# Optimization experiments

Measured on AMD Instinct MI355X. Metric: run time of the kernel, lower is better.

Reference implementation:

```python
import jax, jax.numpy as jnp
import numpy as np

N, E = 50000, 800000
NODE_IN, EDGE_IN, HID, OUT = 64, 16, 64, 32
BN_EPS = 1e-5


def _linear_params(key, fan_in, fan_out):
    kw, kb = jax.random.split(key)
    lim = 1.0 / np.sqrt(fan_in)
    W = jax.random.uniform(kw, (fan_in, fan_out), minval=-lim, maxval=lim, dtype=jnp.float32)
    b = jax.random.uniform(kb, (fan_out,), minval=-lim, maxval=lim, dtype=jnp.float32)
    return W, b


def setup_inputs() -> dict:
    key = jax.random.key(0)
    ks = jax.random.split(key, 8)
    x = jax.random.normal(ks[0], (N, NODE_IN), dtype=jnp.float32)
    edge_index = jax.random.randint(ks[1], (2, E), 0, N, dtype=jnp.int64)
    edge_attr = jax.random.normal(ks[2], (E, EDGE_IN), dtype=jnp.float32)
    # layer 1: message Linear(node_in + edge_in -> hid), self Linear(node_in -> hid)
    W1_msg, b1_msg = _linear_params(ks[3], NODE_IN + EDGE_IN, HID)
    W1_self, b1_self = _linear_params(ks[4], NODE_IN, HID)
    # BatchNorm1d(hidden) params (inference mode: running stats)
    bn_gamma = jnp.ones((HID,), jnp.float32)
    bn_beta = jnp.zeros((HID,), jnp.float32)
    bn_mean = jax.random.normal(ks[5], (HID,), dtype=jnp.float32) * 0.1
    bn_var = jax.random.uniform(ks[6], (HID,), minval=0.5, maxval=1.5, dtype=jnp.float32)
    # layer 2: message Linear(hid + edge_in -> out), self Linear(hid -> out)
    k7, k8 = jax.random.split(ks[7])
    W2_msg, b2_msg = _linear_params(k7, HID + EDGE_IN, OUT)
    W2_self, b2_self = _linear_params(k8, HID, OUT)
    return dict(x=x, edge_index=edge_index, edge_attr=edge_attr,
                W1_msg=W1_msg, b1_msg=b1_msg, W1_self=W1_self, b1_self=b1_self,
                bn_gamma=bn_gamma, bn_beta=bn_beta, bn_mean=bn_mean, bn_var=bn_var,
                W2_msg=W2_msg, b2_msg=b2_msg, W2_self=W2_self, b2_self=b2_self)


def _gnn_layer(x, edge_index, edge_attr, W_msg, b_msg, W_self, b_self):
    # gather source node features per edge, concat edge features, linear, scatter-sum to dst
    src, dst = edge_index[0], edge_index[1]
    m = jnp.concatenate([x[src], edge_attr], axis=-1) @ W_msg + b_msg  # [E, out]
    agg = jax.ops.segment_sum(m, dst, num_segments=x.shape[0])          # [N, out]
    return x @ W_self + b_self + agg


def reference(x, edge_index, edge_attr,
              W1_msg, b1_msg, W1_self, b1_self,
              bn_gamma, bn_beta, bn_mean, bn_var,
              W2_msg, b2_msg, W2_self, b2_self):
    h = _gnn_layer(x, edge_index, edge_attr, W1_msg, b1_msg, W1_self, b1_self)
    # BatchNorm1d (eval mode, running stats) + ReLU; dropout is identity in eval
    h = (h - bn_mean) * jax.lax.rsqrt(bn_var + BN_EPS) * bn_gamma + bn_beta
    h = jax.nn.relu(h)
    return _gnn_layer(h, edge_index, edge_attr, W2_msg, b2_msg, W2_self, b2_self)
```

## Files before the change

kernel.cpp:

```cpp
#include <hip/hip_runtime.h>

#define NN 50000
#define NE 800000
#define NB 6250
#define NT 3125
#define SCB 49
#define NBK 128
#define BNODE 391
#define BCAP 7680
#define SCAP 56

typedef __attribute__((ext_vector_type(8))) short short8x;
typedef __attribute__((ext_vector_type(4))) float f32x4;

#define OFF_CNT   0LL
#define OFF_ROW   ((long long)NN)
#define OFF_RECS  (3LL*NN + 16)
#define OFF_FLAGS (35LL*NN + 16)
#define OFF_BS    (35LL*NN + 32)
#define OFF_BO    (35LL*NN + 96)
#define OFF_PK    (35LL*NN + 160)
#define OFF_FB1S  (35LL*NN + 7840)
#define OFF_FB2S  (35LL*NN + 7904)
#define OFF_F1    (36LL*NN)
#define OFF_F2    (116LL*NN)
#define OFF_Y2B   (164LL*NN)
#define OFF_S2    (180LL*NN)
#define OFF_BCUR  (212LL*NN)

__device__ __forceinline__ float ldf(const void* p, long long i, int bf16) {
  if (bf16) {
    unsigned short u = ((const unsigned short*)p)[i];
    return __uint_as_float(((unsigned)u) << 16);
  }
  return ((const float*)p)[i];
}
__device__ __forceinline__ unsigned short f2bf(float f) {
  unsigned u = __float_as_uint(f);
  unsigned r = (u + 0x7fffu + ((u >> 16) & 1u)) >> 16;
  return (unsigned short)r;
}
__device__ __forceinline__ unsigned pk2(float lo, float hi) {
  return (unsigned)f2bf(lo) | ((unsigned)f2bf(hi) << 16);
}
__device__ __forceinline__ int ldidx(const void* p, long long i, int i64) {
  return i64 ? (int)((const long long*)p)[i] : ((const int*)p)[i];
}
__device__ __forceinline__ float bflo(unsigned u) { return __uint_as_float(u << 16); }
__device__ __forceinline__ float bfhi(unsigned u) { return __uint_as_float(u & 0xffff0000u); }

__global__ void k_detect(const void* ei, const void* x, int* flags) {
  int lane = threadIdx.x & 63;
  const int* p = (const int*)ei;
  int any = 0;
  for (int i = lane; i < 256; i += 64) any |= p[2 * i + 1];
  unsigned long long anyb = __ballot(any != 0);
  const unsigned short* q = (const unsigned short*)x;
  int cnt = 0;
  for (int i = lane; i < 256; i += 64) {
    unsigned short w = q[2 * i];
    int e = (w >> 7) & 0xff;
    if (w == 0 || (e >= 110 && e <= 140)) cnt++;
  }
  for (int m = 1; m < 64; m <<= 1) cnt += __shfl_xor(cnt, m, 64);
  if (lane == 0) {
    flags[0] = (anyb == 0ull) ? 1 : 0;
    flags[1] = (cnt >= 192) ? 1 : 0;
  }
}

__global__ __launch_bounds__(256) void k_prep(
    const void* __restrict__ W1_msg, const void* __restrict__ b1_msg,
    const void* __restrict__ W1_self, const void* __restrict__ b1_self,
    const void* __restrict__ gamma, const void* __restrict__ beta,
    const void* __restrict__ mean, const void* __restrict__ var,
    const void* __restrict__ W2_msg, const void* __restrict__ b2_msg,
    const void* __restrict__ W2_self, const void* __restrict__ b2_self,
    const int* __restrict__ flags, unsigned short* __restrict__ PK,
    float* __restrict__ fb1s, float* __restrict__ fb2s) {
  int bf = flags[1];
  int t0 = blockIdx.x * 256 + threadIdx.x;
  int stride = gridDim.x * 256;
  for (int i = t0; i < 10240; i += stride) {
    int j = i & 7, L = (i >> 3) & 63, t = (i >> 9) & 3, c = i >> 11;
    int k = c * 32 + ((L >> 4) << 3) + j;
    int col = t * 16 + (L & 15);
    float sc = ldf(gamma, col, bf) * rsqrtf(ldf(var, col, bf) + 1e-5f);
    float v;
    if (k < 64) v = ldf(W1_msg, k * 64 + col, bf) * sc;
    else if (k < 128) v = ldf(W1_self, (k - 64) * 64 + col, bf) * sc;
    else if (k < 144) v = ldf(W1_msg, (64 + k - 128) * 64 + col, bf) * sc;
    else if (k == 144) v = ldf(b1_msg, col, bf) * sc;
    else v = 0.0f;
    PK[i] = f2bf(v);
  }
  for (int i = t0; i < 2048; i += stride) {
    int j = i & 7, L = (i >> 3) & 63, t = (i >> 9) & 1, c = i >> 10;
    int k = c * 32 + ((L >> 4) << 3) + j;
    int col = t * 16 + (L & 15);
    PK[10240 + i] = f2bf(ldf(W2_msg, k * 32 + col, bf));
  }
  for (int i = t0; i < 3072; i += stride) {
    int j = i & 7, L = (i >> 3) & 63, t = (i >> 9) & 1, c = i >> 10;
    int k = c * 32 + ((L >> 4) << 3) + j;
    int col = t * 16 + (L & 15);
    float v;
    if (k < 64) v = ldf(W2_self, k * 32 + col, bf);
    else if (k < 80) v = ldf(W2_msg, k * 32 + col, bf);
    else if (k == 80) v = ldf(b2_msg, col, bf);
    else v = 0.0f;
    PK[12288 + i] = f2bf(v);
  }
  for (int i = t0; i < 64; i += stride) {
    float sc = ldf(gamma, i, bf) * rsqrtf(ldf(var, i, bf) + 1e-5f);
    fb1s[i] = ldf(b1_self, i, bf) * sc + ldf(beta, i, bf) - ldf(mean, i, bf) * sc;
  }
  for (int i = t0; i < 32; i += stride) fb2s[i] = ldf(b2_self, i, bf);
}

__global__ __launch_bounds__(256) void k_bin(const void* __restrict__ ei,
                                             const int* __restrict__ flags,
                                             int* __restrict__ bcur,
                                             int2* __restrict__ binbuf) {
  __shared__ int2 stage[NBK][SCAP];
  __shared__ int scnt[NBK];
  __shared__ int gbase[NBK];
  int tid = threadIdx.x;
  for (int i = tid; i < NBK; i += 256) scnt[i] = 0;
  __syncthreads();
  int i64 = flags[0];
  for (long long e0 = (long long)blockIdx.x * 256; e0 < NE;
       e0 += (long long)gridDim.x * 256) {
    long long e = e0 + tid;
    if (e < NE) {
      int src = ldidx(ei, e, i64);
      int dst = ldidx(ei, NE + e, i64);
      int b = dst / BNODE;
      int dl = dst - b * BNODE;
      int2 ent = make_int2(src | (dl << 16), (int)e);
      int pos = atomicAdd(&scnt[b], 1);
      if (pos < SCAP) {
        stage[b][pos] = ent;
      } else {
        int gp = atomicAdd(&bcur[b], 1);
        binbuf[(long long)b * BCAP + gp] = ent;
      }
    }
  }
  __syncthreads();
  if (tid < NBK) {
    int cb = scnt[tid] < SCAP ? scnt[tid] : SCAP;
    gbase[tid] = atomicAdd(&bcur[tid], cb);
  }
  __syncthreads();
  for (int b = 0; b < NBK; ++b) {
    int cb = scnt[b] < SCAP ? scnt[b] : SCAP;
    for (int i = tid; i < cb; i += 256)
      binbuf[(long long)b * BCAP + gbase[b] + i] = stage[b][i];
  }
}

__global__ __launch_bounds__(256) void k_bhist(const int* __restrict__ bcur,
                                               const int2* __restrict__ binbuf,
                                               int* __restrict__ counts) {
  __shared__ int lh[BNODE];
  int b = blockIdx.x;
  int tid = threadIdx.x;
  for (int i = tid; i < BNODE; i += 256) lh[i] = 0;
  __syncthreads();
  int cnt = bcur[b];
  for (int i = tid; i < cnt; i += 256) {
    int dl = (binbuf[(long long)b * BCAP + i].x >> 16) & 0x3FF;
    atomicAdd(&lh[dl], 1);
  }
  __syncthreads();
  int base = b * BNODE;
  int nn = NN - base < BNODE ? NN - base : BNODE;
  for (int i = tid; i < nn; i += 256) counts[base + i] = lh[i];
}

__global__ __launch_bounds__(1024) void k_scanA(const int* __restrict__ counts,
                                                int* __restrict__ bs) {
  __shared__ int sd[1024];
  int t = threadIdx.x;
  int i = blockIdx.x * 1024 + t;
  sd[t] = (i < NN) ? counts[i] : 0;
  __syncthreads();
  for (int off = 512; off > 0; off >>= 1) {
    if (t < off) sd[t] += sd[t + off];
    __syncthreads();
  }
  if (t == 0) bs[blockIdx.x] = sd[0];
}

__global__ void k_scanB(const int* __restrict__ bs, int* __restrict__ bo) {
  int lane = threadIdx.x & 63;
  int v = (lane < SCB) ? bs[lane] : 0;
  int orig = v;
  for (int off = 1; off < 64; off <<= 1) {
    int u = __shfl_up(v, off, 64);
    if (lane >= off) v += u;
  }
  if (lane < SCB) bo[lane] = v - orig;
}

__global__ __launch_bounds__(1024) void k_scanC(const int* __restrict__ counts,
                                                const int* __restrict__ bo,
                                                int* __restrict__ row_ptr) {
  __shared__ int sd[1024];
  int t = threadIdx.x;
  int i = blockIdx.x * 1024 + t;
  int v = (i < NN) ? counts[i] : 0;
  sd[t] = v;
  __syncthreads();
  for (int off = 1; off < 1024; off <<= 1) {
    int u = (t >= off) ? sd[t - off] : 0;
    __syncthreads();
    sd[t] += u;
    __syncthreads();
  }
  int excl = sd[t] - v + bo[blockIdx.x];
  if (i < NN) row_ptr[i] = excl;
  if (i == NN - 1) row_ptr[NN] = excl + v;
}

__global__ __launch_bounds__(256) void k_place(const int* __restrict__ bcur,
                                               const int2* __restrict__ binbuf,
                                               const int* __restrict__ row_ptr,
                                               int2* __restrict__ recs) {
  __shared__ int2 outb[BCAP];
  __shared__ int lcur[BNODE];
  int b = blockIdx.x;
  int tid = threadIdx.x;
  int base = b * BNODE;
  int nn = NN - base < BNODE ? NN - base : BNODE;
  int rbase = row_ptr[base];
  for (int i = tid; i < nn; i += 256) lcur[i] = row_ptr[base + i] - rbase;
  __syncthreads();
  int cnt = bcur[b];
  for (int i = tid; i < cnt; i += 256) {
    int2 ent = binbuf[(long long)b * BCAP + i];
    int dl = (ent.x >> 16) & 0x3FF;
    int p = atomicAdd(&lcur[dl], 1);
    outb[p] = make_int2(ent.x & 0xFFFF, ent.y);
  }
  __syncthreads();
  for (int i = tid; i < cnt; i += 256) recs[rbase + i] = outb[i];
}

__global__ __launch_bounds__(256) void k_gather1(
    const void* __restrict__ x, const void* __restrict__ ea,
    const int* __restrict__ row_ptr, const int2* __restrict__ recs,
    const int* __restrict__ flags, unsigned short* __restrict__ F1,
    unsigned short* __restrict__ F2) {
  int lane = threadIdx.x & 63;
  int g = lane >> 3, c = lane & 7;
  int bf = flags[1];
  long long wid = ((long long)blockIdx.x * blockDim.x + threadIdx.x) >> 6;
  long long nw = ((long long)gridDim.x * blockDim.x) >> 6;
  for (long long b = wid; b < NB; b += nw) {
    int n = (int)(b * 8 + g);
    int beg = row_ptr[n];
    int deg = row_ptr[n + 1] - beg;
    float a0 = 0.f, a1 = 0.f, a2 = 0.f, a3 = 0.f, a4 = 0.f, a5 = 0.f, a6 = 0.f, a7 = 0.f;
    float e0 = 0.f, e1 = 0.f, e2 = 0.f, e3 = 0.f;
    uint4 xw;
    if (bf) {
      const unsigned short* xs = (const unsigned short*)x;
      const unsigned short* es = (const unsigned short*)ea;
      int t = 0;
      for (; t + 4 <= deg; t += 4) {
        int2 r0 = recs[beg + t + 0];
        int2 r1 = recs[beg + t + 1];
        int2 r2 = recs[beg + t + 2];
        int2 r3 = recs[beg + t + 3];
        uint4 w0 = *((const uint4*)(xs + ((long long)r0.x << 6)) + c);
        uint4 w1 = *((const uint4*)(xs + ((long long)r1.x << 6)) + c);
        uint4 w2 = *((const uint4*)(xs + ((long long)r2.x << 6)) + c);
        uint4 w3 = *((const uint4*)(xs + ((long long)r3.x << 6)) + c);
        a0 += bflo(w0.x) + bflo(w1.x) + bflo(w2.x) + bflo(w3.x);
        a1 += bfhi(w0.x) + bfhi(w1.x) + bfhi(w2.x) + bfhi(w3.x);
        a2 += bflo(w0.y) + bflo(w1.y) + bflo(w2.y) + bflo(w3.y);
        a3 += bfhi(w0.y) + bfhi(w1.y) + bfhi(w2.y) + bfhi(w3.y);
        a4 += bflo(w0.z) + bflo(w1.z) + bflo(w2.z) + bflo(w3.z);
        a5 += bfhi(w0.z) + bfhi(w1.z) + bfhi(w2.z) + bfhi(w3.z);
        a6 += bflo(w0.w) + bflo(w1.w) + bflo(w2.w) + bflo(w3.w);
        a7 += bfhi(w0.w) + bfhi(w1.w) + bfhi(w2.w) + bfhi(w3.w);
        if (c < 4) {
          uint2 q0 = *((const uint2*)(es + ((long long)r0.y << 4)) + c);
          uint2 q1 = *((const uint2*)(es + ((long long)r1.y << 4)) + c);
          uint2 q2 = *((const uint2*)(es + ((long long)r2.y << 4)) + c);
          uint2 q3 = *((const uint2*)(es + ((long long)r3.y << 4)) + c);
          e0 += bflo(q0.x) + bflo(q1.x) + bflo(q2.x) + bflo(q3.x);
          e1 += bfhi(q0.x) + bfhi(q1.x) + bfhi(q2.x) + bfhi(q3.x);
          e2 += bflo(q0.y) + bflo(q1.y) + bflo(q2.y) + bflo(q3.y);
          e3 += bfhi(q0.y) + bfhi(q1.y) + bfhi(q2.y) + bfhi(q3.y);
        }
      }
      for (; t < deg; ++t) {
        int2 r = recs[beg + t];
        uint4 w = *((const uint4*)(xs + ((long long)r.x << 6)) + c);
        a0 += bflo(w.x); a1 += bfhi(w.x);
        a2 += bflo(w.y); a3 += bfhi(w.y);
        a4 += bflo(w.z); a5 += bfhi(w.z);
        a6 += bflo(w.w); a7 += bfhi(w.w);
        if (c < 4) {
          uint2 q = *((const uint2*)(es + ((long long)r.y << 4)) + c);
          e0 += bflo(q.x); e1 += bfhi(q.x);
          e2 += bflo(q.y); e3 += bfhi(q.y);
        }
      }
      xw = *((const uint4*)(xs + ((long long)n << 6)) + c);
    } else {
      const float* xf = (const float*)x;
      const float* ef = (const float*)ea;
      for (int t = 0; t < deg; ++t) {
        int2 r = recs[beg + t];
        float4 w0 = *((const float4*)(xf + ((long long)r.x << 6)) + c * 2);
        float4 w1 = *((const float4*)(xf + ((long long)r.x << 6)) + c * 2 + 1);
        a0 += w0.x; a1 += w0.y; a2 += w0.z; a3 += w0.w;
        a4 += w1.x; a5 += w1.y; a6 += w1.z; a7 += w1.w;
        if (c < 4) {
          float4 q = *((const float4*)(ef + ((long long)r.y << 4)) + c);
          e0 += q.x; e1 += q.y; e2 += q.z; e3 += q.w;
        }
      }
      float4 p0 = *((const float4*)(xf + ((long long)n << 6)) + c * 2);
      float4 p1 = *((const float4*)(xf + ((long long)n << 6)) + c * 2 + 1);
      xw = make_uint4(pk2(p0.x, p0.y), pk2(p0.z, p0.w), pk2(p1.x, p1.y), pk2(p1.z, p1.w));
    }
    unsigned short* f1 = F1 + (long long)n * 160;
    unsigned short* f2 = F2 + (long long)n * 96;
    *((uint4*)f1 + c) = make_uint4(pk2(a0, a1), pk2(a2, a3), pk2(a4, a5), pk2(a6, a7));
    *((uint4*)(f1 + 64) + c) = xw;
    if (c < 4) {
      uint2 sp = make_uint2(pk2(e0, e1), pk2(e2, e3));
      *((uint2*)(f1 + 128) + c) = sp;
      *((uint2*)(f2 + 64) + c) = sp;
    }
    if (c == 4) {
      unsigned d = (unsigned)f2bf((float)deg);
      *((uint4*)(f1 + 144)) = make_uint4(d, 0u, 0u, 0u);
      *((uint4*)(f2 + 80)) = make_uint4(d, 0u, 0u, 0u);
    }
    if (c == 5) {
      *((uint4*)(f1 + 152)) = make_uint4(0u, 0u, 0u, 0u);
      *((uint4*)(f2 + 88)) = make_uint4(0u, 0u, 0u, 0u);
    }
  }
}

__global__ __launch_bounds__(256) void k_gemm1(
    const unsigned short* __restrict__ F1, const unsigned short* __restrict__ PK,
    const float* __restrict__ fb1s, unsigned short* __restrict__ F2) {
  int lane = threadIdx.x & 63;
  int wv = threadIdx.x >> 6;
  int m = lane & 15, quad = lane >> 4;
  short8x Bf[20];
#pragma unroll
  for (int s = 0; s < 20; ++s) Bf[s] = *(const short8x*)(PK + (s * 64 + lane) * 8);
  long long gw = (long long)blockIdx.x * 4 + wv;
  long long nw = (long long)gridDim.x * 4;
  for (long long tile = gw; tile < NT; tile += nw) {
    long long n0 = tile * 16;
    const unsigned short* f1 = F1 + (n0 + m) * 160 + quad * 8;
    short8x A[5];
#pragma unroll
    for (int cc = 0; cc < 5; ++cc) A[cc] = *(const short8x*)(f1 + cc * 32);
    f32x4 acc[4];
#pragma unroll
    for (int t = 0; t < 4; ++t) {
      float b = fb1s[t * 16 + m];
      acc[t] = (f32x4){b, b, b, b};
    }
#pragma unroll
    for (int cc = 0; cc < 5; ++cc) {
#pragma unroll
      for (int t = 0; t < 4; ++t)
        acc[t] = __builtin_amdgcn_mfma_f32_16x16x32_bf16(A[cc], Bf[cc * 4 + t], acc[t], 0, 0, 0);
    }
#pragma unroll
    for (int t = 0; t < 4; ++t) {
#pragma unroll
      for (int i = 0; i < 4; ++i) {
        float h = fmaxf(acc[t][i], 0.0f);
        F2[(n0 + quad * 4 + i) * 96 + t * 16 + m] = f2bf(h);
      }
    }
  }
}

__global__ __launch_bounds__(256) void k_gemmY(
    const unsigned short* __restrict__ F2, const unsigned short* __restrict__ PK,
    unsigned short* __restrict__ Y2B) {
  int lane = threadIdx.x & 63;
  int wv = threadIdx.x >> 6;
  int m = lane & 15, quad = lane >> 4;
  short8x Bf[4];
#pragma unroll
  for (int s = 0; s < 4; ++s) Bf[s] = *(const short8x*)(PK + 10240 + (s * 64 + lane) * 8);
  long long gw = (long long)blockIdx.x * 4 + wv;
  long long nw = (long long)gridDim.x * 4;
  for (long long tile = gw; tile < NT; tile += nw) {
    long long n0 = tile * 16;
    const unsigned short* f2 = F2 + (n0 + m) * 96 + quad * 8;
    f32x4 yacc[2];
    yacc[0] = (f32x4){0.f, 0.f, 0.f, 0.f};
    yacc[1] = (f32x4){0.f, 0.f, 0.f, 0.f};
#pragma unroll
    for (int cc = 0; cc < 2; ++cc) {
      short8x Ah = *(const short8x*)(f2 + cc * 32);
#pragma unroll
      for (int t = 0; t < 2; ++t)
        yacc[t] = __builtin_amdgcn_mfma_f32_16x16x32_bf16(Ah, Bf[cc * 2 + t], yacc[t], 0, 0, 0);
    }
#pragma unroll
    for (int t = 0; t < 2; ++t)
#pragma unroll
      for (int i = 0; i < 4; ++i)
        Y2B[(n0 + quad * 4 + i) * 32 + t * 16 + m] = f2bf(yacc[t][i]);
  }
}

__global__ __launch_bounds__(256) void k_gather2(
    const unsigned short* __restrict__ Y2B, const int* __restrict__ row_ptr,
    const int2* __restrict__ recs, float* __restrict__ S2) {
  int lane = threadIdx.x & 63;
  int g = lane >> 3, c = lane & 7;
  long long wid = ((long long)blockIdx.x * blockDim.x + threadIdx.x) >> 6;
  long long nw = ((long long)gridDim.x * blockDim.x) >> 6;
  for (long long b = wid; b < NB; b += nw) {
    int n = (int)(b * 8 + g);
    int beg = row_ptr[n];
    int deg = row_ptr[n + 1] - beg;
    float s0 = 0.f, s1 = 0.f, s2 = 0.f, s3 = 0.f;
    int t = 0;
    for (; t + 4 <= deg; t += 4) {
      int2 r0 = recs[beg + t + 0];
      int2 r1 = recs[beg + t + 1];
      int2 r2 = recs[beg + t + 2];
      int2 r3 = recs[beg + t + 3];
      uint2 q0 = *((const uint2*)(Y2B + (long long)r0.x * 32) + c);
      uint2 q1 = *((const uint2*)(Y2B + (long long)r1.x * 32) + c);
      uint2 q2 = *((const uint2*)(Y2B + (long long)r2.x * 32) + c);
      uint2 q3 = *((const uint2*)(Y2B + (long long)r3.x * 32) + c);
      s0 += bflo(q0.x) + bflo(q1.x) + bflo(q2.x) + bflo(q3.x);
      s1 += bfhi(q0.x) + bfhi(q1.x) + bfhi(q2.x) + bfhi(q3.x);
      s2 += bflo(q0.y) + bflo(q1.y) + bflo(q2.y) + bflo(q3.y);
      s3 += bfhi(q0.y) + bfhi(q1.y) + bfhi(q2.y) + bfhi(q3.y);
    }
    for (; t < deg; ++t) {
      int2 r = recs[beg + t];
      uint2 q = *((const uint2*)(Y2B + (long long)r.x * 32) + c);
      s0 += bflo(q.x); s1 += bfhi(q.x);
      s2 += bflo(q.y); s3 += bfhi(q.y);
    }
    *(float4*)(S2 + (long long)n * 32 + c * 4) = make_float4(s0, s1, s2, s3);
  }
}

__global__ __launch_bounds__(256) void k_gemm2(
    const unsigned short* __restrict__ F2, const unsigned short* __restrict__ PK,
    const float* __restrict__ fb2s, const float* __restrict__ S2,
    const int* __restrict__ flags, void* __restrict__ out) {
  int lane = threadIdx.x & 63;
  int wv = threadIdx.x >> 6;
  int m = lane & 15, quad = lane >> 4;
  int bf = flags[1];
  short8x Bf[6];
#pragma unroll
  for (int s = 0; s < 6; ++s) Bf[s] = *(const short8x*)(PK + 12288 + (s * 64 + lane) * 8);
  long long gw = (long long)blockIdx.x * 4 + wv;
  long long nw = (long long)gridDim.x * 4;
  for (long long tile = gw; tile < NT; tile += nw) {
    long long n0 = tile * 16;
    const unsigned short* f2 = F2 + (n0 + m) * 96 + quad * 8;
    short8x A[3];
#pragma unroll
    for (int cc = 0; cc < 3; ++cc) A[cc] = *(const short8x*)(f2 + cc * 32);
    f32x4 acc[2];
#pragma unroll
    for (int t = 0; t < 2; ++t) {
      float b = fb2s[t * 16 + m];
#pragma unroll
      for (int i = 0; i < 4; ++i)
        acc[t][i] = b + S2[(n0 + quad * 4 + i) * 32 + t * 16 + m];
    }
#pragma unroll
    for (int cc = 0; cc < 3; ++cc) {
#pragma unroll
      for (int t = 0; t < 2; ++t)
        acc[t] = __builtin_amdgcn_mfma_f32_16x16x32_bf16(A[cc], Bf[cc * 2 + t], acc[t], 0, 0, 0);
    }
#pragma unroll
    for (int t = 0; t < 2; ++t) {
#pragma unroll
      for (int i = 0; i < 4; ++i) {
        long long idx = (n0 + quad * 4 + i) * 32 + t * 16 + m;
        if (bf) ((unsigned short*)out)[idx] = f2bf(acc[t][i]);
        else ((float*)out)[idx] = acc[t][i];
      }
    }
  }
}

extern "C" void kernel_launch(void* const* d_in, const int* in_sizes, int n_in,
                              void* d_out, int out_size, void* d_ws, size_t ws_size,
                              hipStream_t stream) {
  const void* x = d_in[0];
  const void* ei = d_in[1];
  const void* ea = d_in[2];
  const void* W1_msg = d_in[3];
  const void* b1_msg = d_in[4];
  const void* W1_self = d_in[5];
  const void* b1_self = d_in[6];
  const void* gamma = d_in[7];
  const void* beta = d_in[8];
  const void* mean = d_in[9];
  const void* var = d_in[10];
  const void* W2_msg = d_in[11];
  const void* b2_msg = d_in[12];
  const void* W2_self = d_in[13];
  const void* b2_self = d_in[14];

  float* ws = (float*)d_ws;
  int* counts = (int*)(ws + OFF_CNT);
  int* row_ptr = (int*)(ws + OFF_ROW);
  int2* recs = (int2*)(ws + OFF_RECS);
  int* flags = (int*)(ws + OFF_FLAGS);
  int* bs = (int*)(ws + OFF_BS);
  int* bo = (int*)(ws + OFF_BO);
  unsigned short* PK = (unsigned short*)(ws + OFF_PK);
  float* fb1s = ws + OFF_FB1S;
  float* fb2s = ws + OFF_FB2S;
  unsigned short* F1 = (unsigned short*)(ws + OFF_F1);
  int2* binbuf = (int2*)(ws + OFF_F1);
  unsigned short* F2 = (unsigned short*)(ws + OFF_F2);
  unsigned short* Y2B = (unsigned short*)(ws + OFF_Y2B);
  float* S2 = ws + OFF_S2;
  int* bcur = (int*)(ws + OFF_BCUR);

  hipLaunchKernelGGL(k_detect, dim3(1), dim3(64), 0, stream, ei, x, flags);
  hipMemsetAsync(bcur, 0, NBK * sizeof(int), stream);
  hipLaunchKernelGGL(k_prep, dim3(64), dim3(256), 0, stream, W1_msg, b1_msg, W1_self,
                     b1_self, gamma, beta, mean, var, W2_msg, b2_msg, W2_self, b2_self,
                     flags, PK, fb1s, fb2s);

  hipLaunchKernelGGL(k_bin, dim3(256), dim3(256), 0, stream, ei, flags, bcur, binbuf);
  hipLaunchKernelGGL(k_bhist, dim3(NBK), dim3(256), 0, stream, bcur, binbuf, counts);
  hipLaunchKernelGGL(k_scanA, dim3(SCB), dim3(1024), 0, stream, counts, bs);
  hipLaunchKernelGGL(k_scanB, dim3(1), dim3(64), 0, stream, bs, bo);
  hipLaunchKernelGGL(k_scanC, dim3(SCB), dim3(1024), 0, stream, counts, bo, row_ptr);
  hipLaunchKernelGGL(k_place, dim3(NBK), dim3(256), 0, stream, bcur, binbuf, row_ptr,
                     recs);

  int gblocks = (NB + 3) / 4;
  hipLaunchKernelGGL(k_gather1, dim3(gblocks), dim3(256), 0, stream, x, ea, row_ptr,
                     recs, flags, F1, F2);
  int mblocks = (NT + 3) / 4;
  hipLaunchKernelGGL(k_gemm1, dim3(mblocks), dim3(256), 0, stream, F1, PK, fb1s, F2);
  hipLaunchKernelGGL(k_gemmY, dim3(mblocks), dim3(256), 0, stream, F2, PK, Y2B);
  hipLaunchKernelGGL(k_gather2, dim3(gblocks), dim3(256), 0, stream, Y2B, row_ptr, recs,
                     S2);
  hipLaunchKernelGGL(k_gemm2, dim3(mblocks), dim3(256), 0, stream, F2, PK, fb2s, S2,
                     flags, d_out);
}
```

Measured before the change: 251.5 us.

## Fuse gemmY into gemm1 via LDS, prefetch edge records, use nontemporal memory ops

The layer-2 message projection (gemmY) now runs inside k_gemm1: each wave stages its ReLU'd hidden tile in shared memory and applies the MFMA directly, so one launch and a re-read of F2 from global memory go away. Both gather kernels software-pipeline the loading of the next four edge records while the current feature loads are in flight. Many loads and stores become nontemporal. The fused path depends on wave-local LDS ordering enforced only by sched_barrier, and nontemporal hints on data reused by later kernels could reduce cache hits.

```diff
diff --git a/kernel.cpp b/kernel.cpp
--- a/kernel.cpp
+++ b/kernel.cpp
@@ -12,6 +12,9 @@
 
 typedef __attribute__((ext_vector_type(8))) short short8x;
 typedef __attribute__((ext_vector_type(4))) float f32x4;
+typedef __attribute__((ext_vector_type(4))) unsigned uint4e;
+typedef __attribute__((ext_vector_type(2))) unsigned uint2e;
+typedef __attribute__((ext_vector_type(2))) int int2e;
 
 #define OFF_CNT   0LL
 #define OFF_ROW   ((long long)NN)
@@ -264,20 +267,40 @@
     int deg = row_ptr[n + 1] - beg;
     float a0 = 0.f, a1 = 0.f, a2 = 0.f, a3 = 0.f, a4 = 0.f, a5 = 0.f, a6 = 0.f, a7 = 0.f;
     float e0 = 0.f, e1 = 0.f, e2 = 0.f, e3 = 0.f;
-    uint4 xw;
+    uint4e xw;
     if (bf) {
       const unsigned short* xs = (const unsigned short*)x;
       const unsigned short* es = (const unsigned short*)ea;
+      xw = *((const uint4e*)(xs + ((long long)n << 6)) + c);
       int t = 0;
-      for (; t + 4 <= deg; t += 4) {
-        int2 r0 = recs[beg + t + 0];
-        int2 r1 = recs[beg + t + 1];
-        int2 r2 = recs[beg + t + 2];
-        int2 r3 = recs[beg + t + 3];
-        uint4 w0 = *((const uint4*)(xs + ((long long)r0.x << 6)) + c);
-        uint4 w1 = *((const uint4*)(xs + ((long long)r1.x << 6)) + c);
-        uint4 w2 = *((const uint4*)(xs + ((long long)r2.x << 6)) + c);
-        uint4 w3 = *((const uint4*)(xs + ((long long)r3.x << 6)) + c);
+      int2e r0, r1, r2, r3;
+      if (t + 4 <= deg) {
+        const int2e* rp = (const int2e*)(recs + beg);
+        r0 = __builtin_nontemporal_load(rp + 0);
+        r1 = __builtin_nontemporal_load(rp + 1);
+        r2 = __builtin_nontemporal_load(rp + 2);
+        r3 = __builtin_nontemporal_load(rp + 3);
+      }
+      for (; t + 4 <= deg;) {
+        uint4e w0 = *((const uint4e*)(xs + ((long long)r0.x << 6)) + c);
+        uint4e w1 = *((const uint4e*)(xs + ((long long)r1.x << 6)) + c);
+        uint4e w2 = *((const uint4e*)(xs + ((long long)r2.x << 6)) + c);
+        uint4e w3 = *((const uint4e*)(xs + ((long long)r3.x << 6)) + c);
+        uint2e q0, q1, q2, q3;
+        if (c < 4) {
+          q0 = __builtin_nontemporal_load((const uint2e*)(es + ((long long)r0.y << 4)) + c);
+          q1 = __builtin_nontemporal_load((const uint2e*)(es + ((long long)r1.y << 4)) + c);
+          q2 = __builtin_nontemporal_load((const uint2e*)(es + ((long long)r2.y << 4)) + c);
+          q3 = __builtin_nontemporal_load((const uint2e*)(es + ((long long)r3.y << 4)) + c);
+        }
+        int tn = t + 4;
+        if (tn + 4 <= deg) {
+          const int2e* rp = (const int2e*)(recs + beg + tn);
+          r0 = __builtin_nontemporal_load(rp + 0);
+          r1 = __builtin_nontemporal_load(rp + 1);
+          r2 = __builtin_nontemporal_load(rp + 2);
+          r3 = __builtin_nontemporal_load(rp + 3);
+        }
         a0 += bflo(w0.x) + bflo(w1.x) + bflo(w2.x) + bflo(w3.x);
         a1 += bfhi(w0.x) + bfhi(w1.x) + bfhi(w2.x) + bfhi(w3.x);
         a2 += bflo(w0.y) + bflo(w1.y) + bflo(w2.y) + bflo(w3.y);
@@ -287,30 +310,26 @@
         a6 += bflo(w0.w) + bflo(w1.w) + bflo(w2.w) + bflo(w3.w);
         a7 += bfhi(w0.w) + bfhi(w1.w) + bfhi(w2.w) + bfhi(w3.w);
         if (c < 4) {
-          uint2 q0 = *((const uint2*)(es + ((long long)r0.y << 4)) + c);
-          uint2 q1 = *((const uint2*)(es + ((long long)r1.y << 4)) + c);
-          uint2 q2 = *((const uint2*)(es + ((long long)r2.y << 4)) + c);
-          uint2 q3 = *((const uint2*)(es + ((long long)r3.y << 4)) + c);
           e0 += bflo(q0.x) + bflo(q1.x) + bflo(q2.x) + bflo(q3.x);
           e1 += bfhi(q0.x) + bfhi(q1.x) + bfhi(q2.x) + bfhi(q3.x);
           e2 += bflo(q0.y) + bflo(q1.y) + bflo(q2.y) + bflo(q3.y);
           e3 += bfhi(q0.y) + bfhi(q1.y) + bfhi(q2.y) + bfhi(q3.y);
         }
+        t = tn;
       }
       for (; t < deg; ++t) {
-        int2 r = recs[beg + t];
-        uint4 w = *((const uint4*)(xs + ((long long)r.x << 6)) + c);
+        int2e r = __builtin_nontemporal_load((const int2e*)(recs + beg) + t);
+        uint4e w = *((const uint4e*)(xs + ((long long)r.x << 6)) + c);
         a0 += bflo(w.x); a1 += bfhi(w.x);
         a2 += bflo(w.y); a3 += bfhi(w.y);
         a4 += bflo(w.z); a5 += bfhi(w.z);
         a6 += bflo(w.w); a7 += bfhi(w.w);
         if (c < 4) {
-          uint2 q = *((const uint2*)(es + ((long long)r.y << 4)) + c);
+          uint2e q = __builtin_nontemporal_load((const uint2e*)(es + ((long long)r.y << 4)) + c);
           e0 += bflo(q.x); e1 += bfhi(q.x);
           e2 += bflo(q.y); e3 += bfhi(q.y);
         }
       }
-      xw = *((const uint4*)(xs + ((long long)n << 6)) + c);
     } else {
       const float* xf = (const float*)x;
       const float* ef = (const float*)ea;
@@ -327,38 +346,50 @@
       }
       float4 p0 = *((const float4*)(xf + ((long long)n << 6)) + c * 2);
       float4 p1 = *((const float4*)(xf + ((long long)n << 6)) + c * 2 + 1);
-      xw = make_uint4(pk2(p0.x, p0.y), pk2(p0.z, p0.w), pk2(p1.x, p1.y), pk2(p1.z, p1.w));
+      xw.x = pk2(p0.x, p0.y); xw.y = pk2(p0.z, p0.w);
+      xw.z = pk2(p1.x, p1.y); xw.w = pk2(p1.z, p1.w);
     }
     unsigned short* f1 = F1 + (long long)n * 160;
     unsigned short* f2 = F2 + (long long)n * 96;
-    *((uint4*)f1 + c) = make_uint4(pk2(a0, a1), pk2(a2, a3), pk2(a4, a5), pk2(a6, a7));
-    *((uint4*)(f1 + 64) + c) = xw;
+    uint4e o1;
+    o1.x = pk2(a0, a1); o1.y = pk2(a2, a3); o1.z = pk2(a4, a5); o1.w = pk2(a6, a7);
+    __builtin_nontemporal_store(o1, (uint4e*)f1 + c);
+    __builtin_nontemporal_store(xw, (uint4e*)(f1 + 64) + c);
     if (c < 4) {
-      uint2 sp = make_uint2(pk2(e0, e1), pk2(e2, e3));
-      *((uint2*)(f1 + 128) + c) = sp;
-      *((uint2*)(f2 + 64) + c) = sp;
+      uint2e sp;
+      sp.x = pk2(e0, e1); sp.y = pk2(e2, e3);
+      __builtin_nontemporal_store(sp, (uint2e*)(f1 + 128) + c);
+      __builtin_nontemporal_store(sp, (uint2e*)(f2 + 64) + c);
     }
     if (c == 4) {
       unsigned d = (unsigned)f2bf((float)deg);
-      *((uint4*)(f1 + 144)) = make_uint4(d, 0u, 0u, 0u);
-      *((uint4*)(f2 + 80)) = make_uint4(d, 0u, 0u, 0u);
+      uint4e dv = {d, 0u, 0u, 0u};
+      __builtin_nontemporal_store(dv, (uint4e*)(f1 + 144));
+      __builtin_nontemporal_store(dv, (uint4e*)(f2 + 80));
     }
     if (c == 5) {
-      *((uint4*)(f1 + 152)) = make_uint4(0u, 0u, 0u, 0u);
-      *((uint4*)(f2 + 88)) = make_uint4(0u, 0u, 0u, 0u);
+      uint4e zv = {0u, 0u, 0u, 0u};
+      __builtin_nontemporal_store(zv, (uint4e*)(f1 + 152));
+      __builtin_nontemporal_store(zv, (uint4e*)(f2 + 88));
     }
   }
 }
 
 __global__ __launch_bounds__(256) void k_gemm1(
     const unsigned short* __restrict__ F1, const unsigned short* __restrict__ PK,
-    const float* __restrict__ fb1s, unsigned short* __restrict__ F2) {
+    const float* __restrict__ fb1s, unsigned short* __restrict__ F2,
+    unsigned short* __restrict__ Y2B) {
+  __shared__ unsigned short hsh[4][16 * 72];
   int lane = threadIdx.x & 63;
   int wv = threadIdx.x >> 6;
   int m = lane & 15, quad = lane >> 4;
+  unsigned short* hs = hsh[wv];
   short8x Bf[20];
 #pragma unroll
   for (int s = 0; s < 20; ++s) Bf[s] = *(const short8x*)(PK + (s * 64 + lane) * 8);
+  short8x By[4];
+#pragma unroll
+  for (int s = 0; s < 4; ++s) By[s] = *(const short8x*)(PK + 10240 + (s * 64 + lane) * 8);
   long long gw = (long long)blockIdx.x * 4 + wv;
   long long nw = (long long)gridDim.x * 4;
   for (long long tile = gw; tile < NT; tile += nw) {
@@ -384,41 +415,29 @@
 #pragma unroll
       for (int i = 0; i < 4; ++i) {
         float h = fmaxf(acc[t][i], 0.0f);
-        F2[(n0 + quad * 4 + i) * 96 + t * 16 + m] = f2bf(h);
-      }
-    }
-  }
-}
-
-__global__ __launch_bounds__(256) void k_gemmY(
-    const unsigned short* __restrict__ F2, const unsigned short* __restrict__ PK,
-    unsigned short* __restrict__ Y2B) {
-  int lane = threadIdx.x & 63;
-  int wv = threadIdx.x >> 6;
-  int m = lane & 15, quad = lane >> 4;
-  short8x Bf[4];
-#pragma unroll
-  for (int s = 0; s < 4; ++s) Bf[s] = *(const short8x*)(PK + 10240 + (s * 64 + lane) * 8);
-  long long gw = (long long)blockIdx.x * 4 + wv;
-  long long nw = (long long)gridDim.x * 4;
-  for (long long tile = gw; tile < NT; tile += nw) {
-    long long n0 = tile * 16;
-    const unsigned short* f2 = F2 + (n0 + m) * 96 + quad * 8;
+        unsigned short us = f2bf(h);
+        __builtin_nontemporal_store(us, &F2[(n0 + quad * 4 + i) * 96 + t * 16 + m]);
+        hs[(quad * 4 + i) * 72 + t * 16 + m] = us;
+      }
+    }
+    __builtin_amdgcn_sched_barrier(0);
     f32x4 yacc[2];
     yacc[0] = (f32x4){0.f, 0.f, 0.f, 0.f};
     yacc[1] = (f32x4){0.f, 0.f, 0.f, 0.f};
 #pragma unroll
     for (int cc = 0; cc < 2; ++cc) {
-      short8x Ah = *(const short8x*)(f2 + cc * 32);
+      short8x Ah = *(const short8x*)(hs + m * 72 + cc * 32 + quad * 8);
 #pragma unroll
       for (int t = 0; t < 2; ++t)
-        yacc[t] = __builtin_amdgcn_mfma_f32_16x16x32_bf16(Ah, Bf[cc * 2 + t], yacc[t], 0, 0, 0);
-    }
-#pragma unroll
-    for (int t = 0; t < 2; ++t)
+        yacc[t] = __builtin_amdgcn_mfma_f32_16x16x32_bf16(Ah, By[cc * 2 + t], yacc[t], 0, 0, 0);
+    }
+#pragma unroll
+    for (int t = 0; t < 2; ++t) {
 #pragma unroll
       for (int i = 0; i < 4; ++i)
         Y2B[(n0 + quad * 4 + i) * 32 + t * 16 + m] = f2bf(yacc[t][i]);
+    }
+    __builtin_amdgcn_sched_barrier(0);
   }
 }
 
@@ -435,27 +454,41 @@
     int deg = row_ptr[n + 1] - beg;
     float s0 = 0.f, s1 = 0.f, s2 = 0.f, s3 = 0.f;
     int t = 0;
-    for (; t + 4 <= deg; t += 4) {
-      int2 r0 = recs[beg + t + 0];
-      int2 r1 = recs[beg + t + 1];
-      int2 r2 = recs[beg + t + 2];
-      int2 r3 = recs[beg + t + 3];
-      uint2 q0 = *((const uint2*)(Y2B + (long long)r0.x * 32) + c);
-      uint2 q1 = *((const uint2*)(Y2B + (long long)r1.x * 32) + c);
-      uint2 q2 = *((const uint2*)(Y2B + (long long)r2.x * 32) + c);
-      uint2 q3 = *((const uint2*)(Y2B + (long long)r3.x * 32) + c);
+    int2e r0, r1, r2, r3;
+    if (t + 4 <= deg) {
+      const int2e* rp = (const int2e*)(recs + beg);
+      r0 = __builtin_nontemporal_load(rp + 0);
+      r1 = __builtin_nontemporal_load(rp + 1);
+      r2 = __builtin_nontemporal_load(rp + 2);
+      r3 = __builtin_nontemporal_load(rp + 3);
+    }
+    for (; t + 4 <= deg;) {
+      uint2e q0 = *((const uint2e*)(Y2B + (long long)r0.x * 32) + c);
+      uint2e q1 = *((const uint2e*)(Y2B + (long long)r1.x * 32) + c);
+      uint2e q2 = *((const uint2e*)(Y2B + (long long)r2.x * 32) + c);
+      uint2e q3 = *((const uint2e*)(Y2B + (long long)r3.x * 32) + c);
+      int tn = t + 4;
+      if (tn + 4 <= deg) {
+        const int2e* rp = (const int2e*)(recs + beg + tn);
+        r0 = __builtin_nontemporal_load(rp + 0);
+        r1 = __builtin_nontemporal_load(rp + 1);
+        r2 = __builtin_nontemporal_load(rp + 2);
+        r3 = __builtin_nontemporal_load(rp + 3);
+      }
       s0 += bflo(q0.x) + bflo(q1.x) + bflo(q2.x) + bflo(q3.x);
       s1 += bfhi(q0.x) + bfhi(q1.x) + bfhi(q2.x) + bfhi(q3.x);
       s2 += bflo(q0.y) + bflo(q1.y) + bflo(q2.y) + bflo(q3.y);
       s3 += bfhi(q0.y) + bfhi(q1.y) + bfhi(q2.y) + bfhi(q3.y);
+      t = tn;
     }
     for (; t < deg; ++t) {
-      int2 r = recs[beg + t];
-      uint2 q = *((const uint2*)(Y2B + (long long)r.x * 32) + c);
+      int2e r = __builtin_nontemporal_load((const int2e*)(recs + beg) + t);
+      uint2e q = *((const uint2e*)(Y2B + (long long)r.x * 32) + c);
       s0 += bflo(q.x); s1 += bfhi(q.x);
       s2 += bflo(q.y); s3 += bfhi(q.y);
     }
-    *(float4*)(S2 + (long long)n * 32 + c * 4) = make_float4(s0, s1, s2, s3);
+    f32x4 o = {s0, s1, s2, s3};
+    __builtin_nontemporal_store(o, (f32x4*)(S2 + (long long)n * 32 + c * 4));
   }
 }
 
@@ -558,8 +591,8 @@
   hipLaunchKernelGGL(k_gather1, dim3(gblocks), dim3(256), 0, stream, x, ea, row_ptr,
                      recs, flags, F1, F2);
   int mblocks = (NT + 3) / 4;
-  hipLaunchKernelGGL(k_gemm1, dim3(mblocks), dim3(256), 0, stream, F1, PK, fb1s, F2);
-  hipLaunchKernelGGL(k_gemmY, dim3(mblocks), dim3(256), 0, stream, F2, PK, Y2B);
+  hipLaunchKernelGGL(k_gemm1, dim3(mblocks), dim3(256), 0, stream, F1, PK, fb1s, F2,
+                     Y2B);
   hipLaunchKernelGGL(k_gather2, dim3(gblocks), dim3(256), 0, stream, Y2B, row_ptr, recs,
                      S2);
   hipLaunchKernelGGL(k_gemm2, dim3(mblocks), dim3(256), 0, stream, F2, PK, fb2s, S2,
```

Result: slower. 270.3 us (+7.5%).
